# Kernel optimization log

Hardware: AMD Instinct MI355X
Metric: run time of the kernel (lower is better)

Reference implementation:

```python
import jax, jax.numpy as jnp
import numpy as np

BN_EPS = 1e-5

def _bn(x, g, b, m, v):
    # eval-mode BatchNorm1d with running stats
    return (x - m) * jax.lax.rsqrt(v + BN_EPS) * g + b

def _gcn(h, src, dst, norm, W, b, N):
    # PyG GCNConv: out[dst] += norm * (h @ W)[src]; then add bias
    msg = (h @ W)[src] * norm[:, None]
    return jax.ops.segment_sum(msg, dst, num_segments=N) + b

def setup_inputs() -> dict:
    key = jax.random.key(0)
    ks = jax.random.split(key, 24)
    N, E, F = 300000, 3000000, 25
    d = {}
    d['x'] = jax.random.normal(ks[0], (N, F), jnp.float32)
    d['edge_index'] = jax.random.randint(ks[1], (2, E), 0, N, dtype=jnp.int64)
    def lin(k, i, o):
        return jax.random.normal(k, (i, o), jnp.float32) / np.float32(np.sqrt(i))
    # ffn1: Linear(25,100) -> BN(100) -> ReLU -> Dropout -> Linear(100,25) -> BN(25) -> Dropout
    d['W1'] = lin(ks[2], 25, 100); d['b1'] = jnp.zeros((100,), jnp.float32)
    d['g1'] = jnp.ones((100,), jnp.float32); d['beta1'] = jnp.zeros((100,), jnp.float32)
    d['m1'] = jnp.zeros((100,), jnp.float32); d['v1'] = jnp.ones((100,), jnp.float32)
    d['W2'] = lin(ks[3], 100, 25); d['b2'] = jnp.zeros((25,), jnp.float32)
    d['g2'] = jnp.ones((25,), jnp.float32); d['beta2'] = jnp.zeros((25,), jnp.float32)
    d['m2'] = jnp.zeros((25,), jnp.float32); d['v2'] = jnp.ones((25,), jnp.float32)
    # GCN layers actually used in forward
    d['Wc1'] = lin(ks[4], 25, 25); d['bc1'] = jnp.zeros((25,), jnp.float32)
    d['Wc2'] = lin(ks[5], 25, 16); d['bc2'] = jnp.zeros((16,), jnp.float32)
    d['Wc3'] = lin(ks[6], 16, 16); d['bc3'] = jnp.zeros((16,), jnp.float32)
    d['Wc4'] = lin(ks[7], 16, 8);  d['bc4'] = jnp.zeros((8,), jnp.float32)
    d['Wc5'] = lin(ks[8], 8, 4);   d['bc5'] = jnp.zeros((4,), jnp.float32)
    # fc: reshape yields 1200 cols (source's Linear(4800,4) is a bug; use 1200)
    d['Wfc'] = lin(ks[9], 1200, 4); d['bfc'] = jnp.zeros((4,), jnp.float32)
    return d

def reference(x, edge_index, W1, b1, g1, beta1, m1, v1, W2, b2, g2, beta2, m2, v2,
              Wc1, bc1, Wc2, bc2, Wc3, bc3, Wc4, bc4, Wc5, bc5, Wfc, bfc):
    N = x.shape[0]
    # add self-loops and compute symmetric normalization once (shared graph)
    loops = jnp.arange(N, dtype=edge_index.dtype)
    src = jnp.concatenate([edge_index[0], loops])
    dst = jnp.concatenate([edge_index[1], loops])
    deg = jax.ops.segment_sum(jnp.ones_like(dst, jnp.float32), dst, num_segments=N)
    dinv = jnp.where(deg > 0, jax.lax.rsqrt(deg), 0.0)
    norm = dinv[src] * dinv[dst]
    # ffn1 (eval mode: dropout is identity)
    h = _bn(x @ W1 + b1, g1, beta1, m1, v1)
    h = jax.nn.relu(h)
    h = _bn(h @ W2 + b2, g2, beta2, m2, v2)
    # stacked GCN layers
    h = jax.nn.relu(_gcn(h, src, dst, norm, Wc1, bc1, N))
    h = jax.nn.relu(_gcn(h, src, dst, norm, Wc2, bc2, N))
    h = jax.nn.relu(_gcn(h, src, dst, norm, Wc3, bc3, N))
    h = jax.nn.relu(_gcn(h, src, dst, norm, Wc4, bc4, N))
    h = jax.nn.relu(_gcn(h, src, dst, norm, Wc5, bc5, N))
    h = h.reshape(-1, 300 * 4)  # [N/300, 1200]
    return h @ Wfc + bfc
```

## Files before the change

### kernel.cpp

```cpp
#include <hip/hip_runtime.h>

#define BN_EPS 1e-5f
#define ELLW 48
#define BSH2 11
#define NPB 2048
#define MAXBK 160
#define BCAP2 26624

struct PartS {
    int hist[MAXBK];
    int cur[MAXBK];
    int gbase[MAXBK];
    int locstart[MAXBK + 1];
    int sc[256];
    int stage[1024];
};

__global__ __launch_bounds__(256) void k_setup(
    const float* __restrict__ W1, const float* __restrict__ b1,
    const float* __restrict__ g1, const float* __restrict__ be1,
    const float* __restrict__ m1, const float* __restrict__ v1,
    const float* __restrict__ W2, const float* __restrict__ b2,
    const float* __restrict__ g2, const float* __restrict__ be2,
    const float* __restrict__ m2, const float* __restrict__ v2,
    const float* __restrict__ Wc1, float* __restrict__ prep,
    const unsigned int* __restrict__ ei2, int* __restrict__ flag,
    int* __restrict__ gcnt)
{
    int t = threadIdx.x;
    if (blockIdx.x == 1) {
        if (t < MAXBK) gcnt[t] = 0;
        if (t < 64) {
            unsigned int v = ei2[2 * t + 1];
            unsigned long long mask = __ballot(v != 0);
            if (t == 0) flag[0] = (mask == 0ULL) ? 1 : 0;
        }
        return;
    }
    __shared__ float s1[100], bb1[100], s2[25], bb2[25], wc[625];
    if (t < 100) {
        float s = g1[t] * rsqrtf(v1[t] + BN_EPS);
        s1[t] = s; bb1[t] = (b1[t] - m1[t]) * s + be1[t];
    }
    if (t >= 128 && t < 153) {
        int u = t - 128;
        float s = g2[u] * rsqrtf(v2[u] + BN_EPS);
        s2[u] = s; bb2[u] = (b2[u] - m2[u]) * s + be2[u];
    }
    for (int q = t; q < 625; q += 256) wc[q] = Wc1[q];
    __syncthreads();
    for (int q = t; q < 2500; q += 256) {
        int kc = q / 625, r = q % 625;
        int j = r / 25, kk = r % 25;
        int k = kc * 25 + kk;
        prep[q] = W1[j * 100 + k] * s1[k];
    }
    for (int q = t; q < 2500; q += 256) {
        int kc = q / 625, r = q % 625;
        int kk = r / 25, j = r % 25;
        int k = kc * 25 + kk;
        float acc = 0.0f;
        for (int m = 0; m < 25; ++m) acc += W2[k * 25 + m] * s2[m] * wc[m * 25 + j];
        prep[2500 + q] = acc;
    }
    if (t < 100) prep[5000 + t] = bb1[t];
    if (t >= 128 && t < 153) {
        int j = t - 128;
        float acc = 0.0f;
        for (int m = 0; m < 25; ++m) acc += bb2[m] * wc[m * 25 + j];
        prep[5104 + j] = acc;
    }
}

__global__ __launch_bounds__(256, 4) void k_ffnpart(
    const float* __restrict__ prep, const float* __restrict__ x,
    float* __restrict__ T,
    const int* __restrict__ ei, const int* __restrict__ flag,
    int* __restrict__ gcnt, int* __restrict__ bdata,
    int nFfn, int N, int E)
{
    __shared__ char smem_raw[sizeof(PartS)];
    int t = threadIdx.x;

    if ((int)blockIdx.x < nFfn) {
        int n = (int)blockIdx.x * 256 + t;
        if (n >= N) return;

        float xi[25];
#pragma unroll
        for (int j = 0; j < 25; ++j) xi[j] = x[(size_t)n * 25 + j];

        float o[25];
#pragma unroll
        for (int j = 0; j < 25; ++j) o[j] = 0.0f;

#pragma unroll 1
        for (int kc = 0; kc < 4; ++kc) {
            const float* __restrict__ w1c = prep + kc * 625;
            const float* __restrict__ w2c = prep + 2500 + kc * 625;
            const float* __restrict__ b1c = prep + 5000 + kc * 25;
            float hm[25];
#pragma unroll
            for (int kk = 0; kk < 25; ++kk) hm[kk] = b1c[kk];
#pragma unroll
            for (int j = 0; j < 25; ++j) {
                float xv = xi[j];
#pragma unroll
                for (int kk = 0; kk < 25; ++kk) hm[kk] += xv * w1c[j * 25 + kk];
            }
#pragma unroll
            for (int kk = 0; kk < 25; ++kk) {
                float r = fmaxf(hm[kk], 0.0f);
#pragma unroll
                for (int j = 0; j < 25; ++j) o[j] += r * w2c[kk * 25 + j];
            }
        }

        float o32[32];
#pragma unroll
        for (int j = 0; j < 25; ++j) o32[j] = o[j] + prep[5104 + j];
#pragma unroll
        for (int j = 25; j < 32; ++j) o32[j] = 0.0f;
        float4* T4 = (float4*)(T + (size_t)n * 32);
#pragma unroll
        for (int q = 0; q < 8; ++q)
            T4[q] = make_float4(o32[4 * q], o32[4 * q + 1], o32[4 * q + 2], o32[4 * q + 3]);
    } else {
        PartS& S = *reinterpret_cast<PartS*>(smem_raw);
        int blockBase = ((int)blockIdx.x - nFfn) * 1024;
        int blockCnt = E - blockBase; if (blockCnt > 1024) blockCnt = 1024; if (blockCnt < 0) blockCnt = 0;

        for (int i = t; i < MAXBK; i += 256) S.hist[i] = 0;
        __syncthreads();

        bool w64 = (flag[0] != 0);
        int e = blockBase + t * 4;
        int s[4], d[4];
        int cnt = 0;
        if (e < E) {
            cnt = E - e; if (cnt > 4) cnt = 4;
            if (cnt == 4) {
                if (w64) {
                    const int4* ps = (const int4*)(ei + (size_t)2 * e);
                    int4 a = ps[0], b = ps[1];
                    s[0] = a.x; s[1] = a.z; s[2] = b.x; s[3] = b.z;
                    const int4* pd = (const int4*)(ei + (size_t)2 * ((size_t)E + e));
                    int4 c = pd[0], f = pd[1];
                    d[0] = c.x; d[1] = c.z; d[2] = f.x; d[3] = f.z;
                } else {
                    int4 a = *(const int4*)(ei + e);
                    s[0] = a.x; s[1] = a.y; s[2] = a.z; s[3] = a.w;
                    int4 c = *(const int4*)(ei + (size_t)E + e);
                    d[0] = c.x; d[1] = c.y; d[2] = c.z; d[3] = c.w;
                }
            } else {
                for (int i = 0; i < cnt; ++i) {
                    if (w64) { s[i] = ei[(size_t)2 * (e + i)]; d[i] = ei[(size_t)2 * ((size_t)E + e + i)]; }
                    else     { s[i] = ei[e + i];               d[i] = ei[(size_t)E + e + i]; }
                }
            }
        }
        int bk[4], pk[4];
        for (int i = 0; i < cnt; ++i) {
            bk[i] = d[i] >> BSH2;
            pk[i] = (s[i] << BSH2) | (d[i] & (NPB - 1));
            atomicAdd(&S.hist[bk[i]], 1);
        }
        __syncthreads();

        S.sc[t] = (t < MAXBK) ? S.hist[t] : 0;
        __syncthreads();
        for (int off = 1; off < 256; off <<= 1) {
            int xv = (t >= off) ? S.sc[t - off] : 0;
            __syncthreads();
            S.sc[t] += xv;
            __syncthreads();
        }
        if (t < MAXBK) {
            S.locstart[t] = S.sc[t] - S.hist[t];
            S.cur[t] = S.sc[t] - S.hist[t];
            if (S.hist[t] > 0) S.gbase[t] = atomicAdd(&gcnt[t], S.hist[t]);
        }
        if (t == 255) S.locstart[MAXBK] = S.sc[MAXBK - 1];
        __syncthreads();

        for (int i = 0; i < cnt; ++i) {
            int p = atomicAdd(&S.cur[bk[i]], 1);
            S.stage[p] = pk[i];
        }
        __syncthreads();

        for (int sIdx = t; sIdx < blockCnt; sIdx += 256) {
            int lo = 0, hi = MAXBK;
            while (hi - lo > 1) {
                int mid = (lo + hi) >> 1;
                if (S.locstart[mid] <= sIdx) lo = mid; else hi = mid;
            }
            int gp = S.gbase[lo] + (sIdx - S.locstart[lo]);
            if (gp < BCAP2) bdata[(size_t)lo * BCAP2 + gp] = S.stage[sIdx];
        }
    }
}

__global__ __launch_bounds__(256) void k_ell2(
    const int* __restrict__ gcnt, const int* __restrict__ bdata,
    int* __restrict__ ell, float* __restrict__ dinv, int N)
{
    __shared__ int lcnt[NPB];
    int b = blockIdx.x;
    int t = threadIdx.x;
    for (int i = t; i < NPB; i += 256) lcnt[i] = 0;
    __syncthreads();
    int base = b << BSH2;
    int cnt = min(gcnt[b], BCAP2);
    const int* __restrict__ bd = bdata + (size_t)b * BCAP2;
    for (int i = t; i < cnt; i += 256) {
        int v = bd[i];
        int dl = v & (NPB - 1);
        int src = v >> BSH2;
        int pos = atomicAdd(&lcnt[dl], 1);
        if (pos < ELLW - 4)
            ell[(size_t)(base + dl) * ELLW + 4 + pos] = src;
    }
    __syncthreads();
    for (int i = t; i < NPB; i += 256) {
        int n = base + i;
        if (n < N) {
            int c = lcnt[i];
            ell[(size_t)n * ELLW] = c;
            dinv[n] = 1.0f / sqrtf((float)(c + 1));
        }
    }
}

template <int DI, int SI, int DO, int LPN, bool SDV>
__global__ __launch_bounds__(256) void k_layer(
    const int* __restrict__ ell,
    const float* __restrict__ dinv, const float* __restrict__ bias,
    const float* __restrict__ W,
    const float* __restrict__ Tin, float* __restrict__ Tout, int N)
{
    constexpr int SI4 = SI / 4;
    constexpr int DO4 = DO / 4;
    constexpr int PAD = LPN * 4;
    __shared__ float sW[DI * DO];
    __shared__ float sB[PAD];
    int t = threadIdx.x;
    for (int i = t; i < DI * DO; i += 256) sW[i] = W[i];
    for (int i = t; i < PAD; i += 256) sB[i] = (i < DI) ? bias[i] : 0.0f;
    __syncthreads();

    int g = t / LPN;
    int j = t % LPN;
    int n = blockIdx.x * (256 / LPN) + g;
    int nc = (n < N) ? n : (N - 1);
    const int* __restrict__ row = ell + (size_t)nc * ELLW;
    int dg = min(row[0], ELLW - 4);
    if (n >= N) dg = 0;
    float dv = dinv[nc];
    const float4* __restrict__ T4 = (const float4*)Tin;

    float4 a0 = T4[(size_t)nc * SI4 + j];
    if (SDV) { a0.x *= dv; a0.y *= dv; a0.z *= dv; a0.w *= dv; }
    float4 a1 = make_float4(0.f, 0.f, 0.f, 0.f);
    float4 a2 = a1, a3 = a1;
    const int4* __restrict__ rowv = (const int4*)(row + 4);
    int k = 0;
    int4 s4;
    if (k + 3 < dg) s4 = rowv[0];
    for (; k + 3 < dg; k += 4) {
        bool more = (k + 7 < dg);
        int4 nx;
        if (more) nx = rowv[(k >> 2) + 1];
        float4 v0 = T4[(size_t)s4.x * SI4 + j];
        float4 v1 = T4[(size_t)s4.y * SI4 + j];
        float4 v2 = T4[(size_t)s4.z * SI4 + j];
        float4 v3 = T4[(size_t)s4.w * SI4 + j];
        if (SDV) {
            float d0 = dinv[s4.x], d1 = dinv[s4.y], d2 = dinv[s4.z], d3 = dinv[s4.w];
            a0.x += d0 * v0.x; a0.y += d0 * v0.y; a0.z += d0 * v0.z; a0.w += d0 * v0.w;
            a1.x += d1 * v1.x; a1.y += d1 * v1.y; a1.z += d1 * v1.z; a1.w += d1 * v1.w;
            a2.x += d2 * v2.x; a2.y += d2 * v2.y; a2.z += d2 * v2.z; a2.w += d2 * v2.w;
            a3.x += d3 * v3.x; a3.y += d3 * v3.y; a3.z += d3 * v3.z; a3.w += d3 * v3.w;
        } else {
            a0.x += v0.x; a0.y += v0.y; a0.z += v0.z; a0.w += v0.w;
            a1.x += v1.x; a1.y += v1.y; a1.z += v1.z; a1.w += v1.w;
            a2.x += v2.x; a2.y += v2.y; a2.z += v2.z; a2.w += v2.w;
            a3.x += v3.x; a3.y += v3.y; a3.z += v3.z; a3.w += v3.w;
        }
        if (more) s4 = nx;
    }
    for (; k < dg; ++k) {
        int sidx = row[4 + k];
        float4 v = T4[(size_t)sidx * SI4 + j];
        float dd = SDV ? dinv[sidx] : 1.0f;
        a0.x += dd * v.x; a0.y += dd * v.y; a0.z += dd * v.z; a0.w += dd * v.w;
    }
    float ar[4];
    ar[0] = fmaxf(dv * (a0.x + a1.x + a2.x + a3.x) + sB[4 * j + 0], 0.0f);
    ar[1] = fmaxf(dv * (a0.y + a1.y + a2.y + a3.y) + sB[4 * j + 1], 0.0f);
    ar[2] = fmaxf(dv * (a0.z + a1.z + a2.z + a3.z) + sB[4 * j + 2], 0.0f);
    ar[3] = fmaxf(dv * (a0.w + a1.w + a2.w + a3.w) + sB[4 * j + 3], 0.0f);

    int lane = t & 63;
    int base = lane - j;
    int jo = (j < DO4) ? j : 0;
    const float4* __restrict__ sW4 = (const float4*)sW;
    float4 o = make_float4(0.f, 0.f, 0.f, 0.f);
#pragma unroll
    for (int k2 = 0; k2 < DI; ++k2) {
        float av = __shfl(ar[k2 & 3], base + (k2 >> 2));
        float4 w = sW4[k2 * DO4 + jo];
        o.x += av * w.x; o.y += av * w.y; o.z += av * w.z; o.w += av * w.w;
    }
    if (n < N && j < DO4)
        ((float4*)Tout)[(size_t)n * DO4 + j] =
            make_float4(dv * o.x, dv * o.y, dv * o.z, dv * o.w);
}

__global__ __launch_bounds__(256) void k_final(
    const int* __restrict__ ell,
    const float* __restrict__ dinv, const float* __restrict__ bias,
    const float* __restrict__ Tin, float* __restrict__ Tout, int N)
{
    int n = blockIdx.x * 256 + threadIdx.x;
    if (n >= N) return;
    const int* __restrict__ row = ell + (size_t)n * ELLW;
    int dg = min(row[0], ELLW - 4);
    float dv = dinv[n];
    const float4* __restrict__ T4 = (const float4*)Tin;

    float4 a0 = T4[n];
    float4 a1 = make_float4(0.f, 0.f, 0.f, 0.f);
    float4 a2 = a1, a3 = a1;
    const int4* __restrict__ rowv = (const int4*)(row + 4);
    int k = 0;
    int4 s4;
    if (k + 3 < dg) s4 = rowv[0];
    for (; k + 3 < dg; k += 4) {
        bool more = (k + 7 < dg);
        int4 nx;
        if (more) nx = rowv[(k >> 2) + 1];
        float4 v0 = T4[s4.x], v1 = T4[s4.y], v2 = T4[s4.z], v3 = T4[s4.w];
        a0.x += v0.x; a0.y += v0.y; a0.z += v0.z; a0.w += v0.w;
        a1.x += v1.x; a1.y += v1.y; a1.z += v1.z; a1.w += v1.w;
        a2.x += v2.x; a2.y += v2.y; a2.z += v2.z; a2.w += v2.w;
        a3.x += v3.x; a3.y += v3.y; a3.z += v3.z; a3.w += v3.w;
        if (more) s4 = nx;
    }
    for (; k < dg; ++k) {
        float4 v = T4[row[4 + k]];
        a0.x += v.x; a0.y += v.y; a0.z += v.z; a0.w += v.w;
    }
    float4 b = *(const float4*)bias;
    ((float4*)Tout)[n] = make_float4(
        fmaxf(dv * (a0.x + a1.x + a2.x + a3.x) + b.x, 0.0f),
        fmaxf(dv * (a0.y + a1.y + a2.y + a3.y) + b.y, 0.0f),
        fmaxf(dv * (a0.z + a1.z + a2.z + a3.z) + b.z, 0.0f),
        fmaxf(dv * (a0.w + a1.w + a2.w + a3.w) + b.w, 0.0f));
}

__global__ __launch_bounds__(256) void k_fc(
    const float* __restrict__ H, const float* __restrict__ Wfc,
    const float* __restrict__ bfc, float* __restrict__ out)
{
    int r = blockIdx.x;
    int t = threadIdx.x;
    float p0 = 0.f, p1 = 0.f, p2 = 0.f, p3 = 0.f;
    for (int k = t; k < 1200; k += 256) {
        float h = H[(size_t)r * 1200 + k];
        p0 += h * Wfc[k * 4 + 0];
        p1 += h * Wfc[k * 4 + 1];
        p2 += h * Wfc[k * 4 + 2];
        p3 += h * Wfc[k * 4 + 3];
    }
#pragma unroll
    for (int off = 32; off > 0; off >>= 1) {
        p0 += __shfl_down(p0, off);
        p1 += __shfl_down(p1, off);
        p2 += __shfl_down(p2, off);
        p3 += __shfl_down(p3, off);
    }
    __shared__ float red[4][4];
    int w = t >> 6, lane = t & 63;
    if (lane == 0) { red[w][0] = p0; red[w][1] = p1; red[w][2] = p2; red[w][3] = p3; }
    __syncthreads();
    if (t < 4) {
        float s = red[0][t] + red[1][t] + red[2][t] + red[3][t];
        out[r * 4 + t] = s + bfc[t];
    }
}

extern "C" void kernel_launch(void* const* d_in, const int* in_sizes, int n_in,
                              void* d_out, int out_size, void* d_ws, size_t ws_size,
                              hipStream_t stream) {
    const float* x   = (const float*)d_in[0];
    const int*   ei  = (const int*)d_in[1];
    const float* W1  = (const float*)d_in[2];
    const float* b1  = (const float*)d_in[3];
    const float* g1  = (const float*)d_in[4];
    const float* be1 = (const float*)d_in[5];
    const float* m1  = (const float*)d_in[6];
    const float* v1  = (const float*)d_in[7];
    const float* W2  = (const float*)d_in[8];
    const float* b2  = (const float*)d_in[9];
    const float* g2  = (const float*)d_in[10];
    const float* be2 = (const float*)d_in[11];
    const float* m2  = (const float*)d_in[12];
    const float* v2  = (const float*)d_in[13];
    const float* Wc1 = (const float*)d_in[14];
    const float* bc1 = (const float*)d_in[15];
    const float* Wc2 = (const float*)d_in[16];
    const float* bc2 = (const float*)d_in[17];
    const float* Wc3 = (const float*)d_in[18];
    const float* bc3 = (const float*)d_in[19];
    const float* Wc4 = (const float*)d_in[20];
    const float* bc4 = (const float*)d_in[21];
    const float* Wc5 = (const float*)d_in[22];
    const float* bc5 = (const float*)d_in[23];
    const float* Wfc = (const float*)d_in[24];
    const float* bfc = (const float*)d_in[25];

    const int N = in_sizes[0] / 25;
    const int E = in_sizes[1] / 2;
    const int NBUCK = (N + NPB - 1) >> BSH2;

    char* ws = (char*)d_ws;
    size_t off = 0;
    auto alloc = [&](size_t bytes) { size_t o = off; off += (bytes + 255) & ~(size_t)255; return o; };
    size_t o_flag = alloc(256);
    size_t o_gcnt = alloc((size_t)MAXBK * 4);
    size_t o_prep = alloc(6144 * 4);
    size_t o_dinv = alloc((size_t)N * 4);
    size_t o_ell  = alloc((size_t)N * ELLW * 4);
    size_t o_A = alloc((size_t)N * 32 * 4);
    size_t o_B = alloc((size_t)N * 16 * 4);
    (void)alloc(4096);

    int*   flag = (int*)(ws + o_flag);
    int*   gcnt = (int*)(ws + o_gcnt);
    float* prep = (float*)(ws + o_prep);
    float* dinv = (float*)(ws + o_dinv);
    int*   ell  = (int*)(ws + o_ell);
    float* A = (float*)(ws + o_A);
    float* B_ = (float*)(ws + o_B);
    int*   bdata = (int*)B_;

    const int B = 256;
    int gN = (N + B - 1) / B;
    int gF = gN;
    int gP = (E + 1023) / 1024;

    k_setup<<<2, B, 0, stream>>>(W1, b1, g1, be1, m1, v1, W2, b2, g2, be2, m2, v2,
                                 Wc1, prep, (const unsigned int*)ei, flag, gcnt);
    k_ffnpart<<<gF + gP, B, 0, stream>>>(prep, x, A, ei, flag, gcnt, bdata, gF, N, E);
    k_ell2<<<NBUCK, B, 0, stream>>>(gcnt, bdata, ell, dinv, N);

    k_layer<25, 32, 16, 8, true><<<(N * 8 + B - 1) / B, B, 0, stream>>>(ell, dinv, bc1, Wc2, A, B_, N);
    k_layer<16, 16, 16, 4, false><<<(N * 4 + B - 1) / B, B, 0, stream>>>(ell, dinv, bc2, Wc3, B_, A, N);
    k_layer<16, 16, 8, 4, false><<<(N * 4 + B - 1) / B, B, 0, stream>>>(ell, dinv, bc3, Wc4, A, B_, N);
    k_layer<8, 8, 4, 2, false><<<(N * 2 + B - 1) / B, B, 0, stream>>>(ell, dinv, bc4, Wc5, B_, A, N);
    k_final<<<gN, B, 0, stream>>>(ell, dinv, bc5, A, B_, N);
    k_fc<<<1000, B, 0, stream>>>(B_, Wfc, bfc, (float*)d_out);
}
```

Measured before the change: 480.5 us.

## Halve dst-bucket width, stage FFN weights in LDS, skip padded GCN lanes

```diff
diff --git a/kernel.cpp b/kernel.cpp
--- a/kernel.cpp
+++ b/kernel.cpp
@@ -2,10 +2,10 @@
 
 #define BN_EPS 1e-5f
 #define ELLW 48
-#define BSH2 11
-#define NPB 2048
-#define MAXBK 160
-#define BCAP2 26624
+#define BSH2 10
+#define NPB 1024
+#define MAXBK 320
+#define BCAP2 13312
 
 struct PartS {
     int hist[MAXBK];
@@ -15,6 +15,7 @@
     int sc[256];
     int stage[1024];
 };
+#define FFN_LDS_FLOATS 5760
 
 __global__ __launch_bounds__(256) void k_setup(
     const float* __restrict__ W1, const float* __restrict__ b1,
@@ -29,7 +30,7 @@
 {
     int t = threadIdx.x;
     if (blockIdx.x == 1) {
-        if (t < MAXBK) gcnt[t] = 0;
+        for (int i = t; i < MAXBK; i += 256) gcnt[i] = 0;
         if (t < 64) {
             unsigned int v = ei2[2 * t + 1];
             unsigned long long mask = __ballot(v != 0);
@@ -49,26 +50,30 @@
     }
     for (int q = t; q < 625; q += 256) wc[q] = Wc1[q];
     __syncthreads();
-    for (int q = t; q < 2500; q += 256) {
-        int kc = q / 625, r = q % 625;
-        int j = r / 25, kk = r % 25;
-        int k = kc * 25 + kk;
-        prep[q] = W1[j * 100 + k] * s1[k];
-    }
-    for (int q = t; q < 2500; q += 256) {
-        int kc = q / 625, r = q % 625;
-        int kk = r / 25, j = r % 25;
-        int k = kc * 25 + kk;
+    for (int q = t; q < 2800; q += 256) {
+        int kc = q / 700, r = q % 700;
+        int j = r / 28, kk = r % 28;
+        prep[q] = (kk < 25) ? W1[j * 100 + kc * 25 + kk] * s1[kc * 25 + kk] : 0.0f;
+    }
+    for (int q = t; q < 2800; q += 256) {
+        int kc = q / 700, r = q % 700;
+        int kk = r / 28, j = r % 28;
         float acc = 0.0f;
-        for (int m = 0; m < 25; ++m) acc += W2[k * 25 + m] * s2[m] * wc[m * 25 + j];
-        prep[2500 + q] = acc;
-    }
-    if (t < 100) prep[5000 + t] = bb1[t];
+        if (j < 25) {
+            int k = kc * 25 + kk;
+            for (int m = 0; m < 25; ++m) acc += W2[k * 25 + m] * s2[m] * wc[m * 25 + j];
+        }
+        prep[2800 + q] = acc;
+    }
+    for (int q = t; q < 112; q += 256) {
+        int kc = q / 28, kk = q % 28;
+        prep[5600 + q] = (kk < 25) ? bb1[kc * 25 + kk] : 0.0f;
+    }
     if (t >= 128 && t < 153) {
         int j = t - 128;
         float acc = 0.0f;
         for (int m = 0; m < 25; ++m) acc += bb2[m] * wc[m * 25 + j];
-        prep[5104 + j] = acc;
+        prep[5712 + j] = acc;
     }
 }
 
@@ -79,10 +84,14 @@
     int* __restrict__ gcnt, int* __restrict__ bdata,
     int nFfn, int N, int E)
 {
-    __shared__ char smem_raw[sizeof(PartS)];
+    __shared__ char smem_raw[FFN_LDS_FLOATS * 4 > sizeof(PartS) ? FFN_LDS_FLOATS * 4 : sizeof(PartS)];
     int t = threadIdx.x;
 
     if ((int)blockIdx.x < nFfn) {
+        float* __restrict__ L = (float*)smem_raw;
+        for (int q = t; q < 5737; q += 256) L[q] = prep[q];
+        __syncthreads();
+
         int n = (int)blockIdx.x * 256 + t;
         if (n >= N) return;
 
@@ -96,29 +105,31 @@
 
 #pragma unroll 1
         for (int kc = 0; kc < 4; ++kc) {
-            const float* __restrict__ w1c = prep + kc * 625;
-            const float* __restrict__ w2c = prep + 2500 + kc * 625;
-            const float* __restrict__ b1c = prep + 5000 + kc * 25;
+            const float* __restrict__ w1c = L + kc * 700;
+            const float* __restrict__ w2c = L + 2800 + kc * 700;
+            const float* __restrict__ b1c = L + 5600 + kc * 28;
             float hm[25];
 #pragma unroll
             for (int kk = 0; kk < 25; ++kk) hm[kk] = b1c[kk];
 #pragma unroll
             for (int j = 0; j < 25; ++j) {
                 float xv = xi[j];
-#pragma unroll
-                for (int kk = 0; kk < 25; ++kk) hm[kk] += xv * w1c[j * 25 + kk];
+                const float* __restrict__ wr = w1c + j * 28;
+#pragma unroll
+                for (int kk = 0; kk < 25; ++kk) hm[kk] += xv * wr[kk];
             }
 #pragma unroll
             for (int kk = 0; kk < 25; ++kk) {
                 float r = fmaxf(hm[kk], 0.0f);
-#pragma unroll
-                for (int j = 0; j < 25; ++j) o[j] += r * w2c[kk * 25 + j];
+                const float* __restrict__ wr = w2c + kk * 28;
+#pragma unroll
+                for (int j = 0; j < 25; ++j) o[j] += r * wr[j];
             }
         }
 
         float o32[32];
 #pragma unroll
-        for (int j = 0; j < 25; ++j) o32[j] = o[j] + prep[5104 + j];
+        for (int j = 0; j < 25; ++j) o32[j] = o[j] + L[5712 + j];
 #pragma unroll
         for (int j = 25; j < 32; ++j) o32[j] = 0.0f;
         float4* T4 = (float4*)(T + (size_t)n * 32);
@@ -168,7 +179,7 @@
         }
         __syncthreads();
 
-        S.sc[t] = (t < MAXBK) ? S.hist[t] : 0;
+        S.sc[t] = (t < MAXBK / 2) ? S.hist[2 * t] + S.hist[2 * t + 1] : 0;
         __syncthreads();
         for (int off = 1; off < 256; off <<= 1) {
             int xv = (t >= off) ? S.sc[t - off] : 0;
@@ -176,12 +187,17 @@
             S.sc[t] += xv;
             __syncthreads();
         }
-        if (t < MAXBK) {
-            S.locstart[t] = S.sc[t] - S.hist[t];
-            S.cur[t] = S.sc[t] - S.hist[t];
-            if (S.hist[t] > 0) S.gbase[t] = atomicAdd(&gcnt[t], S.hist[t]);
-        }
-        if (t == 255) S.locstart[MAXBK] = S.sc[MAXBK - 1];
+        if (t < MAXBK / 2) {
+            int ip = S.sc[t];
+            int h0 = S.hist[2 * t], h1 = S.hist[2 * t + 1];
+            int ls0 = ip - h1 - h0;
+            int ls1 = ip - h1;
+            S.locstart[2 * t] = ls0;  S.cur[2 * t] = ls0;
+            S.locstart[2 * t + 1] = ls1;  S.cur[2 * t + 1] = ls1;
+            if (h0 > 0) S.gbase[2 * t] = atomicAdd(&gcnt[2 * t], h0);
+            if (h1 > 0) S.gbase[2 * t + 1] = atomicAdd(&gcnt[2 * t + 1], h1);
+        }
+        if (t == 255) S.locstart[MAXBK] = S.sc[255];
         __syncthreads();
 
         for (int i = 0; i < cnt; ++i) {
@@ -257,6 +273,7 @@
     const int* __restrict__ row = ell + (size_t)nc * ELLW;
     int dg = min(row[0], ELLW - 4);
     if (n >= N) dg = 0;
+    if (4 * j >= DI) dg = 0;
     float dv = dinv[nc];
     const float4* __restrict__ T4 = (const float4*)Tin;
 
```

After: 535.8 us. 1.12x slower.

## Halve partition bucket size, interleave FFN and partition blocks, skip padded lanes

Applied to the files above, without the earlier changes.

```diff
diff --git a/kernel.cpp b/kernel.cpp
--- a/kernel.cpp
+++ b/kernel.cpp
@@ -2,10 +2,10 @@
 
 #define BN_EPS 1e-5f
 #define ELLW 48
-#define BSH2 11
-#define NPB 2048
-#define MAXBK 160
-#define BCAP2 26624
+#define BSH2 10
+#define NPB 1024
+#define MAXBK 320
+#define BCAP2 13312
 
 struct PartS {
     int hist[MAXBK];
@@ -29,7 +29,7 @@
 {
     int t = threadIdx.x;
     if (blockIdx.x == 1) {
-        if (t < MAXBK) gcnt[t] = 0;
+        for (int i = t; i < MAXBK; i += 256) gcnt[i] = 0;
         if (t < 64) {
             unsigned int v = ei2[2 * t + 1];
             unsigned long long mask = __ballot(v != 0);
@@ -77,13 +77,17 @@
     float* __restrict__ T,
     const int* __restrict__ ei, const int* __restrict__ flag,
     int* __restrict__ gcnt, int* __restrict__ bdata,
-    int nFfn, int N, int E)
+    int nFfn, int nTot, int N, int E)
 {
     __shared__ char smem_raw[sizeof(PartS)];
     int t = threadIdx.x;
-
-    if ((int)blockIdx.x < nFfn) {
-        int n = (int)blockIdx.x * 256 + t;
+    int bid = (int)blockIdx.x;
+    int fb  = (int)(((long long)bid * nFfn) / nTot);
+    int fb1 = (int)(((long long)(bid + 1) * nFfn) / nTot);
+    bool isFfn = (fb1 > fb);
+
+    if (isFfn) {
+        int n = fb * 256 + t;
         if (n >= N) return;
 
         float xi[25];
@@ -127,7 +131,8 @@
             T4[q] = make_float4(o32[4 * q], o32[4 * q + 1], o32[4 * q + 2], o32[4 * q + 3]);
     } else {
         PartS& S = *reinterpret_cast<PartS*>(smem_raw);
-        int blockBase = ((int)blockIdx.x - nFfn) * 1024;
+        int pb = bid - fb;
+        int blockBase = pb * 1024;
         int blockCnt = E - blockBase; if (blockCnt > 1024) blockCnt = 1024; if (blockCnt < 0) blockCnt = 0;
 
         for (int i = t; i < MAXBK; i += 256) S.hist[i] = 0;
@@ -168,7 +173,7 @@
         }
         __syncthreads();
 
-        S.sc[t] = (t < MAXBK) ? S.hist[t] : 0;
+        S.sc[t] = (t < MAXBK / 2) ? S.hist[2 * t] + S.hist[2 * t + 1] : 0;
         __syncthreads();
         for (int off = 1; off < 256; off <<= 1) {
             int xv = (t >= off) ? S.sc[t - off] : 0;
@@ -176,12 +181,17 @@
             S.sc[t] += xv;
             __syncthreads();
         }
-        if (t < MAXBK) {
-            S.locstart[t] = S.sc[t] - S.hist[t];
-            S.cur[t] = S.sc[t] - S.hist[t];
-            if (S.hist[t] > 0) S.gbase[t] = atomicAdd(&gcnt[t], S.hist[t]);
-        }
-        if (t == 255) S.locstart[MAXBK] = S.sc[MAXBK - 1];
+        if (t < MAXBK / 2) {
+            int ip = S.sc[t];
+            int h0 = S.hist[2 * t], h1 = S.hist[2 * t + 1];
+            int ls0 = ip - h1 - h0;
+            int ls1 = ip - h1;
+            S.locstart[2 * t] = ls0;  S.cur[2 * t] = ls0;
+            S.locstart[2 * t + 1] = ls1;  S.cur[2 * t + 1] = ls1;
+            if (h0 > 0) S.gbase[2 * t] = atomicAdd(&gcnt[2 * t], h0);
+            if (h1 > 0) S.gbase[2 * t + 1] = atomicAdd(&gcnt[2 * t + 1], h1);
+        }
+        if (t == 255) S.locstart[MAXBK] = S.sc[255];
         __syncthreads();
 
         for (int i = 0; i < cnt; ++i) {
@@ -257,6 +267,7 @@
     const int* __restrict__ row = ell + (size_t)nc * ELLW;
     int dg = min(row[0], ELLW - 4);
     if (n >= N) dg = 0;
+    if (4 * j >= DI) dg = 0;
     float dv = dinv[nc];
     const float4* __restrict__ T4 = (const float4*)Tin;
 
@@ -450,10 +461,11 @@
     int gN = (N + B - 1) / B;
     int gF = gN;
     int gP = (E + 1023) / 1024;
+    int gT = gF + gP;
 
     k_setup<<<2, B, 0, stream>>>(W1, b1, g1, be1, m1, v1, W2, b2, g2, be2, m2, v2,
                                  Wc1, prep, (const unsigned int*)ei, flag, gcnt);
-    k_ffnpart<<<gF + gP, B, 0, stream>>>(prep, x, A, ei, flag, gcnt, bdata, gF, N, E);
+    k_ffnpart<<<gT, B, 0, stream>>>(prep, x, A, ei, flag, gcnt, bdata, gF, gT, N, E);
     k_ell2<<<NBUCK, B, 0, stream>>>(gcnt, bdata, ell, dinv, N);
 
     k_layer<25, 32, 16, 8, true><<<(N * 8 + B - 1) / B, B, 0, stream>>>(ell, dinv, bc1, Wc2, A, B_, N);
```

Result: slower. 497.7 us (+3.6%).
